# Kernel tuning notes

Measured on AMD Instinct MI355X. Metric: run time of the kernel, lower is better.

Reference implementation:

```python
import jax, jax.numpy as jnp
import numpy as np
from jax import lax

NEG = -10000.0


def setup_inputs() -> dict:
    key = jax.random.key(0)
    ks = jax.random.split(key, 16)
    T, V, E, H, NT = 2048, 50000, 512, 512, 48  # H = per-direction hidden (hidden_dim//2)
    start, end = NT - 2, NT - 1

    def rn(k, shape, scale=0.05):
        return jax.random.normal(k, shape, jnp.float32) * scale

    words = jax.random.randint(ks[0], (T,), 0, V)
    embed = rn(ks[1], (V, E), 0.1)
    Wih_f = rn(ks[2], (4 * H, E)); Whh_f = rn(ks[3], (4 * H, H))
    bih_f = rn(ks[4], (4 * H,));   bhh_f = rn(ks[5], (4 * H,))
    Wih_b = rn(ks[6], (4 * H, E)); Whh_b = rn(ks[7], (4 * H, H))
    bih_b = rn(ks[8], (4 * H,));   bhh_b = rn(ks[9], (4 * H,))
    W_out = rn(ks[10], (NT, 2 * H)); b_out = rn(ks[11], (NT,))
    transitions = jax.random.normal(ks[12], (NT, NT), jnp.float32)
    # match __init__: no transition into START, none out of END
    transitions = transitions.at[start, :].set(NEG).at[:, end].set(NEG)
    h0 = rn(ks[13], (2, H), 1.0)  # [fwd, bwd] initial hidden (torch.randn in init_hidden)
    c0 = rn(ks[14], (2, H), 1.0)
    return dict(words=words, embed=embed,
                Wih_f=Wih_f, Whh_f=Whh_f, bih_f=bih_f, bhh_f=bhh_f,
                Wih_b=Wih_b, Whh_b=Whh_b, bih_b=bih_b, bhh_b=bhh_b,
                W_out=W_out, b_out=b_out, transitions=transitions,
                h0=h0, c0=c0, start_tag=start, end_tag=end)


def _lstm_dir(x, h0, c0, Wih, Whh, bih, bhh, reverse):
    # x: [T, E]. Precompute input contribution for all steps (one big GEMM).
    xW = x @ Wih.T + (bih + bhh)  # [T, 4H]

    def step(carry, g_in):
        h, c = carry
        g = g_in + h @ Whh.T  # [4H]
        i, f, gg, o = jnp.split(g, 4)
        i = jax.nn.sigmoid(i); f = jax.nn.sigmoid(f)
        gg = jnp.tanh(gg);     o = jax.nn.sigmoid(o)
        c = f * c + i * gg
        h = o * jnp.tanh(c)
        return (h, c), h

    _, hs = lax.scan(step, (h0, c0), xW, reverse=reverse)
    return hs  # [T, H], aligned with input time order


def reference(words, embed, Wih_f, Whh_f, bih_f, bhh_f,
              Wih_b, Whh_b, bih_b, bhh_b,
              W_out, b_out, transitions, h0, c0, start_tag, end_tag):
    x = embed[words]  # [T, E]
    hf = _lstm_dir(x, h0[0], c0[0], Wih_f, Whh_f, bih_f, bhh_f, reverse=False)
    hb = _lstm_dir(x, h0[1], c0[1], Wih_b, Whh_b, bih_b, bhh_b, reverse=True)
    frames = jnp.concatenate([hf, hb], axis=-1) @ W_out.T + b_out  # [T, NT] emissions

    nt = transitions.shape[0]
    tT = transitions.T  # tT[from, to]
    alpha0 = jnp.full((nt,), NEG, frames.dtype).at[start_tag].set(0.0)

    def vstep(alpha, frame):
        # smat[i, j] = alpha[i] + frame[j] + transitions[j, i]
        smat = alpha[:, None] + frame[None, :] + tT
        return smat.max(axis=0), jnp.argmax(smat, axis=0)

    alpha, backtrace = lax.scan(vstep, alpha0, frames)  # backtrace: [T, NT]
    final = alpha + transitions[end_tag]
    best_last = jnp.argmax(final)
    score = final[best_last]

    def back(tag, bp):
        prev = bp[tag]
        return prev, prev

    _, path_head = lax.scan(back, best_last, backtrace[1:], reverse=True)  # [T-1]
    best_path = jnp.concatenate([path_head, best_last[None]])  # [T]
    return score, best_path
```

## Files before the change

kernel.cpp:

```cpp
#include <hip/hip_runtime.h>

#define TT 2048
#define HH 512
#define EE 512
#define NTAGS 48
#define G4 2048
#define NWG 16
#define CANARY 1.0e30f

typedef float f4 __attribute__((ext_vector_type(4)));

#define OFF_XW    0ULL
#define OFF_HCAT  (OFF_XW   + 2ULL*TT*G4*4ULL)
#define OFF_FRM   (OFF_HCAT + (unsigned long long)TT*1024ULL*4ULL)
#define OFF_HBUF  (OFF_FRM  + (unsigned long long)TT*NTAGS*4ULL)
#define OFF_BP    (OFF_HBUF + 2ULL*4ULL*HH*4ULL)

__device__ __forceinline__ float fsig(float x) {
    return __builtin_amdgcn_rcpf(1.f + __expf(-x));
}
__device__ __forceinline__ float ftanh(float x) {
    return 1.f - 2.f*__builtin_amdgcn_rcpf(__expf(2.f*x) + 1.f);
}

__global__ __launch_bounds__(256) void k_xw(
    const int* __restrict__ words, const float* __restrict__ embed,
    const float* __restrict__ WihF, const float* __restrict__ WihB,
    const float* __restrict__ bihF, const float* __restrict__ bhhF,
    const float* __restrict__ bihB, const float* __restrict__ bhhB,
    float* __restrict__ xw, float* __restrict__ hbuf)
{
    const int tid = threadIdx.x;
    const int bx = blockIdx.x, by = blockIdx.y, dir = blockIdx.z;

    if (bx == 0 && by == 0) {
        for (int j = tid; j < 4*HH; j += 256)
            hbuf[dir*4*HH + j] = CANARY;
    }

    const float* Wih = dir ? WihB : WihF;
    const float* bi  = dir ? bihB : bihF;
    const float* bh  = dir ? bhhB : bhhF;

    __shared__ float sa[32][64];
    __shared__ float sb[32][64];
    __shared__ int   wds[64];
    if (tid < 64) wds[tid] = words[by*64 + tid];
    const int tx = tid & 15, ty = tid >> 4;
    float acc[4][4] = {};
    __syncthreads();

    for (int k0 = 0; k0 < EE; k0 += 32) {
        #pragma unroll
        for (int u = 0; u < 2; u++) {
            int idx = tid*2 + u;
            int row = idx >> 3, kq = idx & 7;
            float4 av = *(const float4*)&embed[(size_t)wds[row]*EE + k0 + kq*4];
            float4 bv = *(const float4*)&Wih[(size_t)(bx*64 + row)*EE + k0 + kq*4];
            sa[kq*4+0][row] = av.x; sa[kq*4+1][row] = av.y;
            sa[kq*4+2][row] = av.z; sa[kq*4+3][row] = av.w;
            sb[kq*4+0][row] = bv.x; sb[kq*4+1][row] = bv.y;
            sb[kq*4+2][row] = bv.z; sb[kq*4+3][row] = bv.w;
        }
        __syncthreads();
        #pragma unroll
        for (int k = 0; k < 32; k++) {
            float4 a = *(const float4*)&sa[k][ty*4];
            float4 b = *(const float4*)&sb[k][tx*4];
            acc[0][0] += a.x*b.x; acc[0][1] += a.x*b.y; acc[0][2] += a.x*b.z; acc[0][3] += a.x*b.w;
            acc[1][0] += a.y*b.x; acc[1][1] += a.y*b.y; acc[1][2] += a.y*b.z; acc[1][3] += a.y*b.w;
            acc[2][0] += a.z*b.x; acc[2][1] += a.z*b.y; acc[2][2] += a.z*b.z; acc[2][3] += a.z*b.w;
            acc[3][0] += a.w*b.x; acc[3][1] += a.w*b.y; acc[3][2] += a.w*b.z; acc[3][3] += a.w*b.w;
        }
        __syncthreads();
    }

    float* outp = xw + (size_t)dir*TT*G4;
    const int rbase = bx*64 + tx*4;
    float4 bi4 = *(const float4*)&bi[rbase];
    float4 bh4 = *(const float4*)&bh[rbase];
    float4 bias = make_float4(bi4.x+bh4.x, bi4.y+bh4.y, bi4.z+bh4.z, bi4.w+bh4.w);
    #pragma unroll
    for (int i = 0; i < 4; i++) {
        int t = by*64 + ty*4 + i;
        float4 v = make_float4(acc[i][0]+bias.x, acc[i][1]+bias.y,
                               acc[i][2]+bias.z, acc[i][3]+bias.w);
        *(float4*)&outp[(size_t)t*G4 + rbase] = v;
    }
}

__global__ __launch_bounds__(512, 2) void k_lstm(
    const float* __restrict__ WhhF, const float* __restrict__ WhhB,
    const float* __restrict__ h0, const float* __restrict__ c0,
    const float* __restrict__ xw,
    float* __restrict__ hbuf, float* __restrict__ hcat)
{
    const int bid = blockIdx.x;
    const int dir = bid >> 4;
    const int w   = bid & 15;
    const float* Whh = dir ? WhhB : WhhF;
    const float* xwD = xw + (size_t)dir*TT*G4;
    float* hb = hbuf + dir*4*HH;

    const int tid  = threadIdx.x;
    const int rl   = tid >> 2;
    const int q    = tid & 3;
    const int gate = rl >> 5;
    const int jj   = rl & 31;
    const int row  = gate*HH + w*32 + jj;

    f4 wreg[32];
    {
        const f4* wr = (const f4*)&Whh[(size_t)row*HH + q*128];
        #pragma unroll
        for (int k = 0; k < 32; k++)
            asm volatile("global_load_dwordx4 %0, %1, off"
                         : "=v"(wreg[k]) : "v"(wr + k));
        asm volatile("s_waitcnt vmcnt(0)" ::: "memory");
        __builtin_amdgcn_sched_barrier(0);
    }
    float c = 0.f;
    if (tid < 32) c = c0[dir*HH + w*32 + tid];

    __shared__ __align__(16) float hsh[2064];
    __shared__ float gv[128];

    {
        float hv = h0[dir*HH + tid];
        #pragma unroll
        for (int r = 0; r < 4; r++) hsh[r*516 + tid] = hv;
    }
    __syncthreads();

    const float* hq = &hsh[q*644];

    float xv = 0.f;
    if (q == 0) xv = xwD[(size_t)(dir ? TT-1 : 0)*G4 + row];

    for (int s = 0; s < TT; s++) {
        float p0=0.f,p1=0.f,p2=0.f,p3=0.f;
        #pragma unroll
        for (int k = 0; k < 32; k++) {
            float4 hv = *(const float4*)&hq[4*k];
            p0 += wreg[k].x*hv.x; p1 += wreg[k].y*hv.y;
            p2 += wreg[k].z*hv.z; p3 += wreg[k].w*hv.w;
        }
        float part = (p0+p1)+(p2+p3);
        part += __shfl_xor(part, 1);
        part += __shfl_xor(part, 2);
        if (q == 0) gv[rl] = part + xv;
        __syncthreads();

        const int time = dir ? (TT-1-s) : s;
        if (tid < 32) {
            const int jc = w*32 + tid;
            float gi = gv[tid], gf = gv[32+tid], gg = gv[64+tid], go = gv[96+tid];
            float i_ = fsig(gi);
            float f_ = fsig(gf);
            float g_ = ftanh(gg);
            float o_ = fsig(go);
            c = f_*c + i_*g_;
            float hn = o_*ftanh(c);
            if (s+1 < TT) {
                asm volatile("s_waitcnt vmcnt(0)" ::: "memory");
                __hip_atomic_store(&hb[((s+1)&3)*HH + jc], hn,
                                   __ATOMIC_RELAXED, __HIP_MEMORY_SCOPE_AGENT);
                __hip_atomic_store(&hb[((s+3)&3)*HH + jc], CANARY,
                                   __ATOMIC_RELAXED, __HIP_MEMORY_SCOPE_AGENT);
            }
            hcat[(size_t)time*1024 + dir*HH + jc] = hn;
        }

        if (s+1 < TT) {
            float xv_next = 0.f;
            if (q == 0) xv_next = xwD[(size_t)(dir ? TT-2-s : s+1)*G4 + row];

            const float* addr = &hb[((s+1)&3)*HH + tid];
            float va, vb = CANARY; int guard = 0;
            asm volatile("global_load_dword %0, %1, off sc1"
                         : "=v"(va) : "v"(addr));
            for (;;) {
                asm volatile("global_load_dword %0, %1, off sc1"
                             : "=v"(vb) : "v"(addr));
                asm volatile("s_waitcnt vmcnt(1)" ::: "memory");
                __builtin_amdgcn_sched_barrier(0);
                if (va != CANARY) break;
                asm volatile("global_load_dword %0, %1, off sc1"
                             : "=v"(va) : "v"(addr));
                asm volatile("s_waitcnt vmcnt(1)" ::: "memory");
                __builtin_amdgcn_sched_barrier(0);
                if (vb != CANARY) break;
                if (++guard > (1<<14)) break;
            }
            asm volatile("s_waitcnt vmcnt(0)" ::: "memory");
            __builtin_amdgcn_sched_barrier(0);
            float hv = (va != CANARY) ? va : vb;
            #pragma unroll
            for (int r = 0; r < 4; r++) hsh[r*516 + tid] = hv;
            xv = xv_next;
            __syncthreads();
        }
    }
}

__global__ __launch_bounds__(64) void k_frames(
    const float* __restrict__ hcat, const float* __restrict__ Wout,
    const float* __restrict__ bout, float* __restrict__ frames)
{
    const int t = blockIdx.x, tid = threadIdx.x;
    __shared__ float hrow[1024];
    const float4* src  = (const float4*)&hcat[(size_t)t*1024];
    float4* dst4 = (float4*)hrow;
    #pragma unroll
    for (int u = 0; u < 4; u++) dst4[u*64 + tid] = src[u*64 + tid];
    __syncthreads();
    if (tid < NTAGS) {
        float acc = bout[tid];
        const float4* wr = (const float4*)&Wout[(size_t)tid*1024];
        #pragma unroll 16
        for (int e = 0; e < 256; e++) {
            float4 wv = wr[e];
            float4 hv = dst4[e];
            acc += wv.x*hv.x + wv.y*hv.y + wv.z*hv.z + wv.w*hv.w;
        }
        frames[t*NTAGS + tid] = acc;
    }
}

#define CH 256
__global__ __launch_bounds__(256) void k_viterbi(
    const float* __restrict__ frames, const float* __restrict__ trans,
    const int* __restrict__ startp, const int* __restrict__ endp,
    unsigned char* __restrict__ bp, float* __restrict__ out)
{
    const int tid = threadIdx.x;
    const int grp = tid / NTAGS;
    const int j   = tid % NTAGS;
    __shared__ float alpha[2][NTAGS];
    __shared__ float red[4][NTAGS];
    __shared__ int   redarg[4][NTAGS];
    __shared__ float frbuf[2][NTAGS];
    __shared__ __align__(16) unsigned char bps[CH*NTAGS];
    __shared__ int s_tag;

    float tr[12];
    if (grp < 4) {
        #pragma unroll
        for (int u = 0; u < 12; u++) tr[u] = trans[j*NTAGS + grp*12 + u];
    }
    const int start_tag = *startp;
    if (tid < NTAGS) alpha[0][tid] = (tid == start_tag) ? 0.f : -10000.f;
    const bool is_pf = (tid >= 192 && tid < 192 + NTAGS);
    if (is_pf) frbuf[0][tid-192] = frames[tid-192];
    __syncthreads();

    for (int t = 0; t < TT; t++) {
        float fpre = 0.f;
        if (is_pf && t+1 < TT) fpre = frames[(t+1)*NTAGS + (tid-192)];
        if (grp < 4) {
            float best = -3.0e38f; int barg = 0;
            #pragma unroll
            for (int u = 0; u < 12; u++) {
                float sv = alpha[t&1][grp*12+u] + tr[u];
                if (sv > best) { best = sv; barg = grp*12+u; }
            }
            red[grp][j] = best; redarg[grp][j] = barg;
        }
        __syncthreads();
        if (tid < NTAGS) {
            float b = red[0][tid]; int a = redarg[0][tid];
            #pragma unroll
            for (int g2 = 1; g2 < 4; g2++) {
                float v = red[g2][tid];
                if (v > b) { b = v; a = redarg[g2][tid]; }
            }
            bp[t*NTAGS + tid] = (unsigned char)a;
            alpha[(t+1)&1][tid] = b + frbuf[t&1][tid];
        }
        __syncthreads();
        if (is_pf && t+1 < TT) frbuf[(t+1)&1][tid-192] = fpre;
    }

    if (tid == 0) {
        const int end_tag = *endp;
        float best = -3.0e38f; int bl = 0;
        for (int j2 = 0; j2 < NTAGS; j2++) {
            float v = alpha[0][j2] + trans[end_tag*NTAGS + j2];
            if (v > best) { best = v; bl = j2; }
        }
        out[0] = best;
        out[1 + TT - 1] = (float)bl;
        s_tag = bl;
    }
    __syncthreads();

    for (int base = TT - CH; base >= 0; base -= CH) {
        {
            const float4* srcr = (const float4*)&bp[(size_t)(base + tid)*NTAGS];
            float4* dstr = (float4*)&bps[tid*NTAGS];
            dstr[0] = srcr[0]; dstr[1] = srcr[1]; dstr[2] = srcr[2];
        }
        __syncthreads();
        if (tid == 0) {
            int tag = s_tag;
            const int thi = base + CH - 1;
            const int tlo = (base == 0) ? 1 : base;
            for (int t = thi; t >= tlo; t--) {
                tag = bps[(t - base)*NTAGS + tag];
                out[t] = (float)tag;
            }
            s_tag = tag;
        }
        __syncthreads();
    }
}

extern "C" void kernel_launch(void* const* d_in, const int* in_sizes, int n_in,
                              void* d_out, int out_size, void* d_ws, size_t ws_size,
                              hipStream_t stream)
{
    const int*   words = (const int*)  d_in[0];
    const float* embed = (const float*)d_in[1];
    const float* WihF  = (const float*)d_in[2];
    const float* WhhF  = (const float*)d_in[3];
    const float* bihF  = (const float*)d_in[4];
    const float* bhhF  = (const float*)d_in[5];
    const float* WihB  = (const float*)d_in[6];
    const float* WhhB  = (const float*)d_in[7];
    const float* bihB  = (const float*)d_in[8];
    const float* bhhB  = (const float*)d_in[9];
    const float* Wout  = (const float*)d_in[10];
    const float* bout  = (const float*)d_in[11];
    const float* trans = (const float*)d_in[12];
    const float* h0    = (const float*)d_in[13];
    const float* c0    = (const float*)d_in[14];
    const int*   startp= (const int*)  d_in[15];
    const int*   endp  = (const int*)  d_in[16];

    char* ws = (char*)d_ws;
    float* xw   = (float*)(ws + OFF_XW);
    float* hcat = (float*)(ws + OFF_HCAT);
    float* frm  = (float*)(ws + OFF_FRM);
    float* hbuf = (float*)(ws + OFF_HBUF);
    unsigned char* bp = (unsigned char*)(ws + OFF_BP);

    dim3 g1(32, 32, 2);
    k_xw<<<g1, 256, 0, stream>>>(words, embed, WihF, WihB, bihF, bhhF,
                                 bihB, bhhB, xw, hbuf);
    k_lstm<<<dim3(2*NWG), 512, 0, stream>>>(WhhF, WhhB, h0, c0, xw, hbuf, hcat);
    k_frames<<<dim3(TT), 64, 0, stream>>>(hcat, Wout, bout, frm);
    k_viterbi<<<dim3(1), 256, 0, stream>>>(frm, trans, startp, endp, bp, (float*)d_out);
}
```

Before: 4.819 ms.

## Remap LSTM recurrent matvec so each lane covers four gates over a K-slice

Each thread now holds Whh weights for all four gates of one hidden unit over a 32-wide K slice, so one h load from LDS feeds four gate dot products and LDS read traffic per step drops. The old four-way replicated h copy in shared memory becomes a single padded layout, double-buffered by step parity. The cross-lane reduction grows from 2 to 4 butterfly steps per gate (16 shuffles per thread), which trades LDS bandwidth for shuffle latency on the serial critical path.

```diff
diff --git a/kernel.cpp b/kernel.cpp
--- a/kernel.cpp
+++ b/kernel.cpp
@@ -103,52 +103,64 @@
     float* hb = hbuf + dir*4*HH;
 
     const int tid  = threadIdx.x;
-    const int rl   = tid >> 2;
-    const int q    = tid & 3;
-    const int gate = rl >> 5;
-    const int jj   = rl & 31;
-    const int row  = gate*HH + w*32 + jj;
-
-    f4 wreg[32];
+    const int v    = tid >> 6;
+    const int l    = tid & 63;
+    const int hi   = l >> 4;
+    const int k16  = l & 15;
+    const int loc  = v*4 + hi;
+    const int hidx = w*32 + loc;
+
+    f4 wreg[4][8];
     {
-        const f4* wr = (const f4*)&Whh[(size_t)row*HH + q*128];
-        #pragma unroll
-        for (int k = 0; k < 32; k++)
-            asm volatile("global_load_dwordx4 %0, %1, off"
-                         : "=v"(wreg[k]) : "v"(wr + k));
+        #pragma unroll
+        for (int g = 0; g < 4; g++) {
+            const f4* wr = (const f4*)&Whh[(size_t)(g*HH + hidx)*HH + k16*32];
+            #pragma unroll
+            for (int t = 0; t < 8; t++)
+                asm volatile("global_load_dwordx4 %0, %1, off"
+                             : "=v"(wreg[g][t]) : "v"(wr + t));
+        }
         asm volatile("s_waitcnt vmcnt(0)" ::: "memory");
         __builtin_amdgcn_sched_barrier(0);
     }
     float c = 0.f;
     if (tid < 32) c = c0[dir*HH + w*32 + tid];
 
-    __shared__ __align__(16) float hsh[2064];
+    __shared__ __align__(16) float hsh[2][16*36];
     __shared__ float gv[128];
 
-    {
-        float hv = h0[dir*HH + tid];
-        #pragma unroll
-        for (int r = 0; r < 4; r++) hsh[r*516 + tid] = hv;
-    }
-    __syncthreads();
-
-    const float* hq = &hsh[q*644];
+    hsh[0][(tid>>5)*36 + (tid&31)] = h0[dir*HH + tid];
+    __syncthreads();
 
     float xv = 0.f;
-    if (q == 0) xv = xwD[(size_t)(dir ? TT-1 : 0)*G4 + row];
+    if (k16 < 4) xv = xwD[(size_t)(dir ? TT-1 : 0)*G4 + k16*HH + hidx];
 
     for (int s = 0; s < TT; s++) {
-        float p0=0.f,p1=0.f,p2=0.f,p3=0.f;
-        #pragma unroll
-        for (int k = 0; k < 32; k++) {
-            float4 hv = *(const float4*)&hq[4*k];
-            p0 += wreg[k].x*hv.x; p1 += wreg[k].y*hv.y;
-            p2 += wreg[k].z*hv.z; p3 += wreg[k].w*hv.w;
-        }
-        float part = (p0+p1)+(p2+p3);
-        part += __shfl_xor(part, 1);
-        part += __shfl_xor(part, 2);
-        if (q == 0) gv[rl] = part + xv;
+        const float* hc = &hsh[s & 1][k16*36];
+        f4 p = {0.f, 0.f, 0.f, 0.f};
+        #pragma unroll
+        for (int t = 0; t < 8; t++) {
+            float4 hv = *(const float4*)&hc[4*t];
+            p.x += wreg[0][t].x*hv.x; p.x += wreg[0][t].y*hv.y;
+            p.x += wreg[0][t].z*hv.z; p.x += wreg[0][t].w*hv.w;
+            p.y += wreg[1][t].x*hv.x; p.y += wreg[1][t].y*hv.y;
+            p.y += wreg[1][t].z*hv.z; p.y += wreg[1][t].w*hv.w;
+            p.z += wreg[2][t].x*hv.x; p.z += wreg[2][t].y*hv.y;
+            p.z += wreg[2][t].z*hv.z; p.z += wreg[2][t].w*hv.w;
+            p.w += wreg[3][t].x*hv.x; p.w += wreg[3][t].y*hv.y;
+            p.w += wreg[3][t].z*hv.z; p.w += wreg[3][t].w*hv.w;
+        }
+        #pragma unroll
+        for (int m = 1; m < 16; m <<= 1) {
+            p.x += __shfl_xor(p.x, m);
+            p.y += __shfl_xor(p.y, m);
+            p.z += __shfl_xor(p.z, m);
+            p.w += __shfl_xor(p.w, m);
+        }
+        if (k16 < 4) {
+            float sv = (k16 == 0) ? p.x : (k16 == 1) ? p.y : (k16 == 2) ? p.z : p.w;
+            gv[k16*32 + loc] = sv + xv;
+        }
         __syncthreads();
 
         const int time = dir ? (TT-1-s) : s;
@@ -173,7 +185,8 @@
 
         if (s+1 < TT) {
             float xv_next = 0.f;
-            if (q == 0) xv_next = xwD[(size_t)(dir ? TT-2-s : s+1)*G4 + row];
+            if (k16 < 4)
+                xv_next = xwD[(size_t)(dir ? TT-2-s : s+1)*G4 + k16*HH + hidx];
 
             const float* addr = &hb[((s+1)&3)*HH + tid];
             float va, vb = CANARY; int guard = 0;
@@ -195,8 +208,7 @@
             asm volatile("s_waitcnt vmcnt(0)" ::: "memory");
             __builtin_amdgcn_sched_barrier(0);
             float hv = (va != CANARY) ? va : vb;
-            #pragma unroll
-            for (int r = 0; r < 4; r++) hsh[r*516 + tid] = hv;
+            hsh[(s+1)&1][(tid>>5)*36 + (tid&31)] = hv;
             xv = xv_next;
             __syncthreads();
         }
```

After: 4.992 ms. 3.6% more time.

## Rewrite Viterbi forward pass as single-wavefront shuffle-based recurrence

Applied to the files above, without the earlier changes.

The Viterbi kernel now runs in a single 64-thread wavefront. Each lane keeps its full transition row in registers and reads alpha from other lanes with shuffles, so the per-step shared-memory reductions and the two __syncthreads per timestep are gone. Each lane does four parallel max/argmax chains of 12 elements, then merges them, and frames are prefetched one step ahead in a register. The cost is more serial work per lane (48 compares instead of 12) and more register pressure, in exchange for removing barrier latency from the 2048-step critical path.

```diff
diff --git a/kernel.cpp b/kernel.cpp
--- a/kernel.cpp
+++ b/kernel.cpp
@@ -228,64 +228,62 @@
 }
 
 #define CH 256
-__global__ __launch_bounds__(256) void k_viterbi(
+__global__ __launch_bounds__(64) void k_viterbi(
     const float* __restrict__ frames, const float* __restrict__ trans,
     const int* __restrict__ startp, const int* __restrict__ endp,
     unsigned char* __restrict__ bp, float* __restrict__ out)
 {
-    const int tid = threadIdx.x;
-    const int grp = tid / NTAGS;
-    const int j   = tid % NTAGS;
-    __shared__ float alpha[2][NTAGS];
-    __shared__ float red[4][NTAGS];
-    __shared__ int   redarg[4][NTAGS];
-    __shared__ float frbuf[2][NTAGS];
+    const int j = threadIdx.x;
+    __shared__ float afinal[NTAGS];
     __shared__ __align__(16) unsigned char bps[CH*NTAGS];
     __shared__ int s_tag;
 
-    float tr[12];
-    if (grp < 4) {
-        #pragma unroll
-        for (int u = 0; u < 12; u++) tr[u] = trans[j*NTAGS + grp*12 + u];
-    }
+    float tr[NTAGS];
+    float alpha = -3.0e38f;
     const int start_tag = *startp;
-    if (tid < NTAGS) alpha[0][tid] = (tid == start_tag) ? 0.f : -10000.f;
-    const bool is_pf = (tid >= 192 && tid < 192 + NTAGS);
-    if (is_pf) frbuf[0][tid-192] = frames[tid-192];
-    __syncthreads();
+    if (j < NTAGS) {
+        #pragma unroll
+        for (int i = 0; i < NTAGS; i++) tr[i] = trans[j*NTAGS + i];
+        alpha = (j == start_tag) ? 0.f : -10000.f;
+    }
+    float fcur = (j < NTAGS) ? frames[j] : 0.f;
 
     for (int t = 0; t < TT; t++) {
-        float fpre = 0.f;
-        if (is_pf && t+1 < TT) fpre = frames[(t+1)*NTAGS + (tid-192)];
-        if (grp < 4) {
-            float best = -3.0e38f; int barg = 0;
-            #pragma unroll
-            for (int u = 0; u < 12; u++) {
-                float sv = alpha[t&1][grp*12+u] + tr[u];
-                if (sv > best) { best = sv; barg = grp*12+u; }
-            }
-            red[grp][j] = best; redarg[grp][j] = barg;
-        }
-        __syncthreads();
-        if (tid < NTAGS) {
-            float b = red[0][tid]; int a = redarg[0][tid];
-            #pragma unroll
-            for (int g2 = 1; g2 < 4; g2++) {
-                float v = red[g2][tid];
-                if (v > b) { b = v; a = redarg[g2][tid]; }
-            }
-            bp[t*NTAGS + tid] = (unsigned char)a;
-            alpha[(t+1)&1][tid] = b + frbuf[t&1][tid];
-        }
-        __syncthreads();
-        if (is_pf && t+1 < TT) frbuf[(t+1)&1][tid-192] = fpre;
-    }
-
-    if (tid == 0) {
+        float fnext = 0.f;
+        if (j < NTAGS && t+1 < TT) fnext = frames[(t+1)*NTAGS + j];
+
+        float b0 = -3.0e38f, b1 = -3.0e38f, b2 = -3.0e38f, b3 = -3.0e38f;
+        int   a0 = 0, a1 = 12, a2 = 24, a3 = 36;
+        #pragma unroll
+        for (int u = 0; u < 12; u++) {
+            float s0 = __shfl(alpha, u)      + tr[u];
+            float s1 = __shfl(alpha, 12 + u) + tr[12 + u];
+            float s2 = __shfl(alpha, 24 + u) + tr[24 + u];
+            float s3 = __shfl(alpha, 36 + u) + tr[36 + u];
+            if (s0 > b0) { b0 = s0; a0 = u; }
+            if (s1 > b1) { b1 = s1; a1 = 12 + u; }
+            if (s2 > b2) { b2 = s2; a2 = 24 + u; }
+            if (s3 > b3) { b3 = s3; a3 = 36 + u; }
+        }
+        float best = b0; int barg = a0;
+        if (b1 > best) { best = b1; barg = a1; }
+        if (b2 > best) { best = b2; barg = a2; }
+        if (b3 > best) { best = b3; barg = a3; }
+
+        if (j < NTAGS) {
+            bp[t*NTAGS + j] = (unsigned char)barg;
+            alpha = best + fcur;
+        }
+        fcur = fnext;
+    }
+    if (j < NTAGS) afinal[j] = alpha;
+    __syncthreads();
+
+    if (j == 0) {
         const int end_tag = *endp;
         float best = -3.0e38f; int bl = 0;
         for (int j2 = 0; j2 < NTAGS; j2++) {
-            float v = alpha[0][j2] + trans[end_tag*NTAGS + j2];
+            float v = afinal[j2] + trans[end_tag*NTAGS + j2];
             if (v > best) { best = v; bl = j2; }
         }
         out[0] = best;
@@ -295,13 +293,15 @@
     __syncthreads();
 
     for (int base = TT - CH; base >= 0; base -= CH) {
-        {
-            const float4* srcr = (const float4*)&bp[(size_t)(base + tid)*NTAGS];
-            float4* dstr = (float4*)&bps[tid*NTAGS];
+        #pragma unroll
+        for (int u = 0; u < 4; u++) {
+            const int row = u*64 + j;
+            const float4* srcr = (const float4*)&bp[(size_t)(base + row)*NTAGS];
+            float4* dstr = (float4*)&bps[row*NTAGS];
             dstr[0] = srcr[0]; dstr[1] = srcr[1]; dstr[2] = srcr[2];
         }
         __syncthreads();
-        if (tid == 0) {
+        if (j == 0) {
             int tag = s_tag;
             const int thi = base + CH - 1;
             const int tlo = (base == 0) ? 1 : base;
@@ -349,5 +349,5 @@
                                  bihB, bhhB, xw, hbuf);
     k_lstm<<<dim3(2*NWG), 512, 0, stream>>>(WhhF, WhhB, h0, c0, xw, hbuf, hcat);
     k_frames<<<dim3(TT), 64, 0, stream>>>(hcat, Wout, bout, frm);
-    k_viterbi<<<dim3(1), 256, 0, stream>>>(frm, trans, startp, endp, bp, (float*)d_out);
-}
+    k_viterbi<<<dim3(1), 64, 0, stream>>>(frm, trans, startp, endp, bp, (float*)d_out);
+}
```

Result: slower. 5.449 ms (+13.1%).

## Fuse input-projection GEMM into persistent LSTM kernel with per-tile readiness counters

Applied to the files above, without the earlier changes.

Merges the input-projection GEMM and the recurrent LSTM into one launch. The first 32 blocks run the recurrence while the remaining blocks compute xW tiles, ordered from both sequence ends, and signal completion through per-tile atomic counters. The recurrent blocks spin on a tile's counter before reading its xW values. This overlaps the GEMM with the start of the serial scan and removes a launch boundary. In exchange it adds a tiny init kernel, spin-waits, and a dependence on the 32 recurrent blocks being co-resident with the GEMM blocks.

```diff
diff --git a/kernel.cpp b/kernel.cpp
--- a/kernel.cpp
+++ b/kernel.cpp
@@ -15,6 +15,7 @@
 #define OFF_FRM   (OFF_HCAT + (unsigned long long)TT*1024ULL*4ULL)
 #define OFF_HBUF  (OFF_FRM  + (unsigned long long)TT*NTAGS*4ULL)
 #define OFF_BP    (OFF_HBUF + 2ULL*4ULL*HH*4ULL)
+#define OFF_TCNT  (OFF_BP   + (unsigned long long)TT*NTAGS)
 
 __device__ __forceinline__ float fsig(float x) {
     return __builtin_amdgcn_rcpf(1.f + __expf(-x));
@@ -23,86 +24,113 @@
     return 1.f - 2.f*__builtin_amdgcn_rcpf(__expf(2.f*x) + 1.f);
 }
 
-__global__ __launch_bounds__(256) void k_xw(
+__global__ __launch_bounds__(256) void k_init(float* __restrict__ hbuf,
+                                              int* __restrict__ tilecnt)
+{
+    const int tid = threadIdx.x;
+    for (int j = tid; j < 2*4*HH; j += 256) hbuf[j] = CANARY;
+    if (tid < 64) tilecnt[tid] = 0;
+}
+
+__global__ __launch_bounds__(512, 2) void k_mega(
     const int* __restrict__ words, const float* __restrict__ embed,
     const float* __restrict__ WihF, const float* __restrict__ WihB,
     const float* __restrict__ bihF, const float* __restrict__ bhhF,
     const float* __restrict__ bihB, const float* __restrict__ bhhB,
-    float* __restrict__ xw, float* __restrict__ hbuf)
-{
-    const int tid = threadIdx.x;
-    const int bx = blockIdx.x, by = blockIdx.y, dir = blockIdx.z;
-
-    if (bx == 0 && by == 0) {
-        for (int j = tid; j < 4*HH; j += 256)
-            hbuf[dir*4*HH + j] = CANARY;
-    }
-
-    const float* Wih = dir ? WihB : WihF;
-    const float* bi  = dir ? bihB : bihF;
-    const float* bh  = dir ? bhhB : bhhF;
-
-    __shared__ float sa[32][64];
-    __shared__ float sb[32][64];
-    __shared__ int   wds[64];
-    if (tid < 64) wds[tid] = words[by*64 + tid];
-    const int tx = tid & 15, ty = tid >> 4;
-    float acc[4][4] = {};
-    __syncthreads();
-
-    for (int k0 = 0; k0 < EE; k0 += 32) {
-        #pragma unroll
-        for (int u = 0; u < 2; u++) {
-            int idx = tid*2 + u;
-            int row = idx >> 3, kq = idx & 7;
-            float4 av = *(const float4*)&embed[(size_t)wds[row]*EE + k0 + kq*4];
-            float4 bv = *(const float4*)&Wih[(size_t)(bx*64 + row)*EE + k0 + kq*4];
-            sa[kq*4+0][row] = av.x; sa[kq*4+1][row] = av.y;
-            sa[kq*4+2][row] = av.z; sa[kq*4+3][row] = av.w;
-            sb[kq*4+0][row] = bv.x; sb[kq*4+1][row] = bv.y;
-            sb[kq*4+2][row] = bv.z; sb[kq*4+3][row] = bv.w;
-        }
-        __syncthreads();
-        #pragma unroll
-        for (int k = 0; k < 32; k++) {
-            float4 a = *(const float4*)&sa[k][ty*4];
-            float4 b = *(const float4*)&sb[k][tx*4];
-            acc[0][0] += a.x*b.x; acc[0][1] += a.x*b.y; acc[0][2] += a.x*b.z; acc[0][3] += a.x*b.w;
-            acc[1][0] += a.y*b.x; acc[1][1] += a.y*b.y; acc[1][2] += a.y*b.z; acc[1][3] += a.y*b.w;
-            acc[2][0] += a.z*b.x; acc[2][1] += a.z*b.y; acc[2][2] += a.z*b.z; acc[2][3] += a.z*b.w;
-            acc[3][0] += a.w*b.x; acc[3][1] += a.w*b.y; acc[3][2] += a.w*b.z; acc[3][3] += a.w*b.w;
-        }
-        __syncthreads();
-    }
-
-    float* outp = xw + (size_t)dir*TT*G4;
-    const int rbase = bx*64 + tx*4;
-    float4 bi4 = *(const float4*)&bi[rbase];
-    float4 bh4 = *(const float4*)&bh[rbase];
-    float4 bias = make_float4(bi4.x+bh4.x, bi4.y+bh4.y, bi4.z+bh4.z, bi4.w+bh4.w);
-    #pragma unroll
-    for (int i = 0; i < 4; i++) {
-        int t = by*64 + ty*4 + i;
-        float4 v = make_float4(acc[i][0]+bias.x, acc[i][1]+bias.y,
-                               acc[i][2]+bias.z, acc[i][3]+bias.w);
-        *(float4*)&outp[(size_t)t*G4 + rbase] = v;
-    }
-}
-
-__global__ __launch_bounds__(512, 2) void k_lstm(
     const float* __restrict__ WhhF, const float* __restrict__ WhhB,
     const float* __restrict__ h0, const float* __restrict__ c0,
-    const float* __restrict__ xw,
-    float* __restrict__ hbuf, float* __restrict__ hcat)
+    float* __restrict__ xw, float* __restrict__ hbuf,
+    float* __restrict__ hcat, int* __restrict__ tilecnt)
 {
     const int bid = blockIdx.x;
+    const int tid = threadIdx.x;
+
+    __shared__ float sa[32][64];
+    __shared__ float sb[2][32][64];
+    __shared__ int   wds[64];
+    __shared__ __align__(16) float hsh[2064];
+    __shared__ float gv[128];
+
+    if (bid >= 32) {
+        const int e    = bid - 32;
+        const int dir  = e & 1;
+        const int xbx  = (e >> 1) & 15;
+        const int byi  = e >> 5;
+        const int by   = (byi & 1) ? (31 - (byi >> 1)) : (byi >> 1);
+        const int half = tid >> 8;
+        const int t8   = tid & 255;
+        const int bxe  = xbx*2 + half;
+
+        const float* Wih = dir ? WihB : WihF;
+        const float* bi  = dir ? bihB : bihF;
+        const float* bh  = dir ? bhhB : bhhF;
+
+        if (tid < 64) wds[tid] = words[by*64 + tid];
+        const int tx = t8 & 15, ty = t8 >> 4;
+        float acc[4][4] = {};
+        __syncthreads();
+
+        for (int k0 = 0; k0 < EE; k0 += 32) {
+            if (tid < 256) {
+                #pragma unroll
+                for (int u = 0; u < 2; u++) {
+                    int idx = tid*2 + u;
+                    int row = idx >> 3, kq = idx & 7;
+                    float4 av = *(const float4*)&embed[(size_t)wds[row]*EE + k0 + kq*4];
+                    sa[kq*4+0][row] = av.x; sa[kq*4+1][row] = av.y;
+                    sa[kq*4+2][row] = av.z; sa[kq*4+3][row] = av.w;
+                }
+            }
+            #pragma unroll
+            for (int u = 0; u < 2; u++) {
+                int idx = t8*2 + u;
+                int row = idx >> 3, kq = idx & 7;
+                float4 bv = *(const float4*)&Wih[(size_t)(bxe*64 + row)*EE + k0 + kq*4];
+                sb[half][kq*4+0][row] = bv.x; sb[half][kq*4+1][row] = bv.y;
+                sb[half][kq*4+2][row] = bv.z; sb[half][kq*4+3][row] = bv.w;
+            }
+            __syncthreads();
+            #pragma unroll
+            for (int k = 0; k < 32; k++) {
+                float4 a = *(const float4*)&sa[k][ty*4];
+                float4 b = *(const float4*)&sb[half][k][tx*4];
+                acc[0][0] += a.x*b.x; acc[0][1] += a.x*b.y; acc[0][2] += a.x*b.z; acc[0][3] += a.x*b.w;
+                acc[1][0] += a.y*b.x; acc[1][1] += a.y*b.y; acc[1][2] += a.y*b.z; acc[1][3] += a.y*b.w;
+                acc[2][0] += a.z*b.x; acc[2][1] += a.z*b.y; acc[2][2] += a.z*b.z; acc[2][3] += a.z*b.w;
+                acc[3][0] += a.w*b.x; acc[3][1] += a.w*b.y; acc[3][2] += a.w*b.z; acc[3][3] += a.w*b.w;
+            }
+            __syncthreads();
+        }
+
+        float* outp = xw + (size_t)dir*TT*G4;
+        const int rbase = bxe*64 + tx*4;
+        float4 bi4 = *(const float4*)&bi[rbase];
+        float4 bh4 = *(const float4*)&bh[rbase];
+        f4 bias = {bi4.x+bh4.x, bi4.y+bh4.y, bi4.z+bh4.z, bi4.w+bh4.w};
+        #pragma unroll
+        for (int i = 0; i < 4; i++) {
+            int t = by*64 + ty*4 + i;
+            f4 v = {acc[i][0]+bias.x, acc[i][1]+bias.y,
+                    acc[i][2]+bias.z, acc[i][3]+bias.w};
+            const float* ad = &outp[(size_t)t*G4 + rbase];
+            asm volatile("global_store_dwordx4 %0, %1, off sc1"
+                         :: "v"(ad), "v"(v) : "memory");
+        }
+        asm volatile("s_waitcnt vmcnt(0)" ::: "memory");
+        __syncthreads();
+        if (tid == 0)
+            __hip_atomic_fetch_add(&tilecnt[dir*32 + by], 1,
+                                   __ATOMIC_RELEASE, __HIP_MEMORY_SCOPE_AGENT);
+        return;
+    }
+
     const int dir = bid >> 4;
     const int w   = bid & 15;
     const float* Whh = dir ? WhhB : WhhF;
     const float* xwD = xw + (size_t)dir*TT*G4;
     float* hb = hbuf + dir*4*HH;
-
-    const int tid  = threadIdx.x;
+    const int* tcnt = &tilecnt[dir*32];
+
     const int rl   = tid >> 2;
     const int q    = tid & 3;
     const int gate = rl >> 5;
@@ -122,9 +150,6 @@
     float c = 0.f;
     if (tid < 32) c = c0[dir*HH + w*32 + tid];
 
-    __shared__ __align__(16) float hsh[2064];
-    __shared__ float gv[128];
-
     {
         float hv = h0[dir*HH + tid];
         #pragma unroll
@@ -134,8 +159,23 @@
 
     const float* hq = &hsh[q*644];
 
+    int lastTile = -1;
     float xv = 0.f;
-    if (q == 0) xv = xwD[(size_t)(dir ? TT-1 : 0)*G4 + row];
+    if (q == 0) {
+        const int t0 = dir ? TT-1 : 0;
+        const int tile = t0 >> 6;
+        for (;;) {
+            int fv = __hip_atomic_load(&tcnt[tile], __ATOMIC_RELAXED,
+                                       __HIP_MEMORY_SCOPE_AGENT);
+            if (fv >= 16) break;
+            __builtin_amdgcn_s_sleep(16);
+        }
+        asm volatile("" ::: "memory");
+        __builtin_amdgcn_sched_barrier(0);
+        lastTile = tile;
+        xv = __hip_atomic_load(&xwD[(size_t)t0*G4 + row], __ATOMIC_RELAXED,
+                               __HIP_MEMORY_SCOPE_AGENT);
+    }
 
     for (int s = 0; s < TT; s++) {
         float p0=0.f,p1=0.f,p2=0.f,p3=0.f;
@@ -173,7 +213,23 @@
 
         if (s+1 < TT) {
             float xv_next = 0.f;
-            if (q == 0) xv_next = xwD[(size_t)(dir ? TT-2-s : s+1)*G4 + row];
+            if (q == 0) {
+                const int tnext = dir ? TT-2-s : s+1;
+                const int tile = tnext >> 6;
+                if (tile != lastTile) {
+                    for (;;) {
+                        int fv = __hip_atomic_load(&tcnt[tile], __ATOMIC_RELAXED,
+                                                   __HIP_MEMORY_SCOPE_AGENT);
+                        if (fv >= 16) break;
+                        __builtin_amdgcn_s_sleep(16);
+                    }
+                    asm volatile("" ::: "memory");
+                    __builtin_amdgcn_sched_barrier(0);
+                    lastTile = tile;
+                }
+                xv_next = __hip_atomic_load(&xwD[(size_t)tnext*G4 + row],
+                                            __ATOMIC_RELAXED, __HIP_MEMORY_SCOPE_AGENT);
+            }
 
             const float* addr = &hb[((s+1)&3)*HH + tid];
             float va, vb = CANARY; int guard = 0;
@@ -190,7 +246,7 @@
                 asm volatile("s_waitcnt vmcnt(1)" ::: "memory");
                 __builtin_amdgcn_sched_barrier(0);
                 if (vb != CANARY) break;
-                if (++guard > (1<<14)) break;
+                if (++guard > (1<<16)) break;
             }
             asm volatile("s_waitcnt vmcnt(0)" ::: "memory");
             __builtin_amdgcn_sched_barrier(0);
@@ -343,11 +399,12 @@
     float* frm  = (float*)(ws + OFF_FRM);
     float* hbuf = (float*)(ws + OFF_HBUF);
     unsigned char* bp = (unsigned char*)(ws + OFF_BP);
-
-    dim3 g1(32, 32, 2);
-    k_xw<<<g1, 256, 0, stream>>>(words, embed, WihF, WihB, bihF, bhhF,
-                                 bihB, bhhB, xw, hbuf);
-    k_lstm<<<dim3(2*NWG), 512, 0, stream>>>(WhhF, WhhB, h0, c0, xw, hbuf, hcat);
+    int* tilecnt = (int*)(ws + OFF_TCNT);
+
+    k_init<<<dim3(1), 256, 0, stream>>>(hbuf, tilecnt);
+    k_mega<<<dim3(32 + 1024), 512, 0, stream>>>(
+        words, embed, WihF, WihB, bihF, bhhF, bihB, bhhB,
+        WhhF, WhhB, h0, c0, xw, hbuf, hcat, tilecnt);
     k_frames<<<dim3(TT), 64, 0, stream>>>(hcat, Wout, bout, frm);
     k_viterbi<<<dim3(1), 256, 0, stream>>>(frm, trans, startp, endp, bp, (float*)d_out);
 }
```

Result: slower. 5.032 ms (+4.4%).
